# Optimization experiments

Hardware: AMD Instinct MI355X
Metric: run time of the kernel (lower is better)

## Reference

```python
import jax, jax.numpy as jnp
import numpy as np

D_MODEL, D_K, D_V, H, GRID = 512, 64, 64, 8, 196
B = 4


def setup_inputs() -> dict:
    key = jax.random.key(0)
    ks = jax.random.split(key, 12)
    s = 0.02
    return {
        "queries": jax.random.normal(ks[0], (B, GRID, D_MODEL), jnp.float32),
        "keys": jax.random.normal(ks[1], (B, GRID, D_MODEL), jnp.float32),
        "values": jax.random.normal(ks[2], (B, GRID, D_MODEL), jnp.float32),
        "Wq": jax.random.normal(ks[3], (H * D_K, D_MODEL), jnp.float32) * s,
        "bq": jnp.zeros((H * D_K,), jnp.float32),
        "Wk": jax.random.normal(ks[4], (H * D_K, D_MODEL), jnp.float32) * s,
        "bk": jnp.zeros((H * D_K,), jnp.float32),
        "Wv": jax.random.normal(ks[5], (H * D_V, D_MODEL), jnp.float32) * s,
        "bv": jnp.zeros((H * D_V,), jnp.float32),
        "Wo": jax.random.normal(ks[6], (D_MODEL, H * D_V), jnp.float32) * s,
        "bo": jnp.zeros((D_MODEL,), jnp.float32),
        "scale": jnp.ones((1, H, GRID, GRID), jnp.float32) / np.sqrt(D_K).astype(np.float32),
    }


def reference(queries, keys, values, Wq, bq, Wk, bk, Wv, bv, Wo, bo, scale):
    b, nq, _ = queries.shape
    nk = values.shape[1]
    # linear projections (torch nn.Linear: x @ W.T + b)
    q_sig = queries @ Wq.T + bq          # (b, nq, h*dk)
    k_p = keys @ Wk.T + bk               # (b, nk, h*dk)
    v_p = values @ Wv.T + bv             # (b, nk, h*dv)
    # elementwise q*k interaction (b, nq, nk, h*dk)
    att_e = q_sig[:, :, None, :] * k_p[:, None, :, :]
    # sigmoid-gated values
    v_g = jax.nn.sigmoid(att_e) * v_p[:, None, :, :]
    v = v_g.reshape(b, nq, nk, H, D_K).transpose(0, 3, 1, 2, 4)      # (b,h,nq,nk,dk)
    att = att_e.reshape(b, nq, nk, H, D_K).transpose(0, 3, 1, 2, 4)  # (b,h,nq,nk,dk)
    att = att.sum(-1) * scale            # (b,h,nq,nk)
    p = jax.nn.softmax(att, axis=-1)     # dropout is identity in eval mode
    # (att.unsqueeze(-2) @ v).squeeze(-2)
    image = jnp.einsum("bhqk,bhqkd->bhqd", p, v)
    image = image.transpose(0, 2, 1, 3).reshape(b, nq, H * D_V)
    out = image @ Wo.T + bo              # (b, nq, d_model)
    out = jax.nn.sigmoid(q_sig * out) * out
    return out
```

## Files before the change

kernel.cpp:

```cpp
#include <hip/hip_runtime.h>
#include <hip/hip_bf16.h>
#include <math.h>

#define NQ 196
#define BATCH 4
#define HD 512
#define NH 8
#define DK 64
#define MROWS 784
#define MPAD 832

typedef __attribute__((ext_vector_type(8))) short short8;
typedef __attribute__((ext_vector_type(4))) short short4v;
typedef __attribute__((ext_vector_type(4))) float float4v;

__device__ __forceinline__ float b2f(short s) {
  return __uint_as_float(((unsigned)(unsigned short)s) << 16);
}
__device__ __forceinline__ short f2b(float x) {
  return __builtin_bit_cast(short, __float2bfloat16(x));
}
__device__ __forceinline__ float fexp2(float x) {
  float r; asm("v_exp_f32 %0, %1" : "=v"(r) : "v"(x)); return r;
}
__device__ __forceinline__ float frcp(float x) {
  float r; asm("v_rcp_f32 %0, %1" : "=v"(r) : "v"(x)); return r;
}
__device__ __forceinline__ void cvt4(float4 v, short4v& hi, short4v& lo) {
  float x[4] = {v.x, v.y, v.z, v.w};
  #pragma unroll
  for (int i = 0; i < 4; ++i) {
    hi[i] = f2b(x[i]);
    lo[i] = f2b(x[i] - b2f(hi[i]));
  }
}
__device__ __forceinline__ void cvt8(float4 v0, float4 v1, short8& hi, short8& lo) {
  short4v h0, l0, h1, l1;
  cvt4(v0, h0, l0); cvt4(v1, h1, l1);
  hi = short8{h0[0],h0[1],h0[2],h0[3],h1[0],h1[1],h1[2],h1[3]};
  lo = short8{l0[0],l0[1],l0[2],l0[3],l1[0],l1[1],l1[2],l1[3]};
}
__device__ __forceinline__ void gload_lds16(const void* g, void* l) {
  __builtin_amdgcn_global_load_lds(
      (const __attribute__((address_space(1))) unsigned int*)g,
      (__attribute__((address_space(3))) unsigned int*)l, 16, 0, 0);
}

struct ProjArgs {
  const float* X[3]; const float* W[3]; const float* bias[3];
  float* Cf[3]; short* Ch[3]; short* Cl[3];
  const float* Wo; short* Woh; short* Wol;
};

__global__ __launch_bounds__(512)
void proj_kernel(ProjArgs a) {
  const int z = blockIdx.z;
  const float* __restrict__ X = a.X[z];
  const float* __restrict__ W = a.W[z];
  const int t = threadIdx.x;
  const int ln = t & 63, lm = ln & 15, quad = ln >> 4;
  const int w = t >> 6, wm = w >> 1, wn = w & 1;
  const int m0 = blockIdx.x << 6, n0 = blockIdx.y << 6;

  __shared__ __align__(16) short smem[32768];

  const int sr = t >> 3;
  const int cg = (t & 7) << 3;
  const int wIdx = sr * 64 + (cg ^ ((sr & 7) << 3));
  const float* gA = X + (size_t)min(m0 + sr, MROWS - 1) * HD;
  const float* gB = W + (size_t)(n0 + sr) * HD;

  float4 ra0, ra1, rb0, rb1;
  float4v acc0 = {0.f,0.f,0.f,0.f}, acc1 = {0.f,0.f,0.f,0.f};
  const int ar = (wm << 4) + lm;
  const int br0 = (wn << 5) + lm, br1 = br0 + 16;
  const int swz = (lm & 7) << 3;

  ra0 = *(const float4*)(gA + cg);     ra1 = *(const float4*)(gA + cg + 4);
  rb0 = *(const float4*)(gB + cg);     rb1 = *(const float4*)(gB + cg + 4);
  {
    short8 hi, lo;
    cvt8(ra0, ra1, hi, lo);
    *(short8*)&smem[0    + wIdx] = hi;  *(short8*)&smem[4096  + wIdx] = lo;
    cvt8(rb0, rb1, hi, lo);
    *(short8*)&smem[8192 + wIdx] = hi;  *(short8*)&smem[12288 + wIdx] = lo;
  }

  for (int kt = 0; kt < 8; ++kt) {
    const int buf = kt & 1;
    __syncthreads();
    if (kt < 7) {
      const int kb = (kt + 1) << 6;
      ra0 = *(const float4*)(gA + kb + cg);  ra1 = *(const float4*)(gA + kb + cg + 4);
      rb0 = *(const float4*)(gB + kb + cg);  rb1 = *(const float4*)(gB + kb + cg + 4);
    }
    const short* Sb = smem + (buf << 14);
    #pragma unroll
    for (int h2 = 0; h2 < 2; ++h2) {
      const int c = (h2 << 5) + (quad << 3);
      const int cs = c ^ swz;
      short8 a_h = *(const short8*)&Sb[         ar  * 64 + cs];
      short8 a_l = *(const short8*)&Sb[4096  +  ar  * 64 + cs];
      short8 b0h = *(const short8*)&Sb[8192  +  br0 * 64 + cs];
      short8 b0l = *(const short8*)&Sb[12288 +  br0 * 64 + cs];
      short8 b1h = *(const short8*)&Sb[8192  +  br1 * 64 + cs];
      short8 b1l = *(const short8*)&Sb[12288 +  br1 * 64 + cs];
      acc0 = __builtin_amdgcn_mfma_f32_16x16x32_bf16(a_h, b0h, acc0, 0,0,0);
      acc0 = __builtin_amdgcn_mfma_f32_16x16x32_bf16(a_h, b0l, acc0, 0,0,0);
      acc0 = __builtin_amdgcn_mfma_f32_16x16x32_bf16(a_l, b0h, acc0, 0,0,0);
      acc1 = __builtin_amdgcn_mfma_f32_16x16x32_bf16(a_h, b1h, acc1, 0,0,0);
      acc1 = __builtin_amdgcn_mfma_f32_16x16x32_bf16(a_h, b1l, acc1, 0,0,0);
      acc1 = __builtin_amdgcn_mfma_f32_16x16x32_bf16(a_l, b1h, acc1, 0,0,0);
    }
    if (kt < 7) {
      short* Nb = smem + ((buf ^ 1) << 14);
      short8 hi, lo;
      cvt8(ra0, ra1, hi, lo);
      *(short8*)&Nb[0    + wIdx] = hi;  *(short8*)&Nb[4096  + wIdx] = lo;
      cvt8(rb0, rb1, hi, lo);
      *(short8*)&Nb[8192 + wIdx] = hi;  *(short8*)&Nb[12288 + wIdx] = lo;
    }
  }

  {
    const float* bias = a.bias[z];
    float* Cf = a.Cf[z]; short* Ch = a.Ch[z]; short* Cl = a.Cl[z];
    #pragma unroll
    for (int nf = 0; nf < 2; ++nf) {
      const float4v av = nf ? acc1 : acc0;
      const int n = n0 + (wn << 5) + (nf << 4) + lm;
      const float bv = bias[n];
      #pragma unroll
      for (int r = 0; r < 4; ++r) {
        const int m = m0 + (wm << 4) + (quad << 2) + r;
        const float c = av[r] + bv;
        Cf[(size_t)m * HD + n] = c;
        if (Ch) {
          const short hi = f2b(c);
          Ch[(size_t)m * HD + n] = hi;
          Cl[(size_t)m * HD + n] = f2b(c - b2f(hi));
        }
      }
    }
  }

  if (z == 2) {
    const int lin = blockIdx.y * 13 + blockIdx.x;
    if (lin < 64) {
      const size_t off = (size_t)lin * 4096 + (size_t)t * 8;
      float4 v0 = *(const float4*)(a.Wo + off);
      float4 v1 = *(const float4*)(a.Wo + off + 4);
      short8 hi, lo; cvt8(v0, v1, hi, lo);
      *(short8*)(a.Woh + off) = hi;
      *(short8*)(a.Wol + off) = lo;
    }
  }
}

__global__ __launch_bounds__(512)
void attn_fused(const short* __restrict__ qsh, const short* __restrict__ qsl,
                const short* __restrict__ ksh, const short* __restrict__ ksl,
                const float* __restrict__ qsg, const float* __restrict__ kpg,
                const float* __restrict__ vpg, const float* __restrict__ scg,
                short* __restrict__ imgh, short* __restrict__ imgl) {
  const int q0 = blockIdx.x * 16;
  const int h  = blockIdx.y;
  const int b  = blockIdx.z;
  const int t  = threadIdx.x;
  const int w = t >> 6, ln = t & 63;
  const int lm = ln & 15, quad = ln >> 4;
  const float L2E = 1.4426950408889634f;

  __shared__ __align__(16) float S[16][212];
  __shared__ float R2[2][16][64];

  const size_t abase = ((size_t)(b * NQ) + q0 + lm) * HD + h * DK + (quad << 3);
  short8 ah0 = *(const short8*)(qsh + abase);
  short8 ah1 = *(const short8*)(qsh + abase + 32);
  short8 al0 = *(const short8*)(qsl + abase);
  short8 al1 = *(const short8*)(qsl + abase + 32);

  for (int nt = w; nt < 13; nt += 8) {
    const size_t bbase = ((size_t)(b * NQ) + nt * 16 + lm) * HD + h * DK + (quad << 3);
    short8 bh0 = *(const short8*)(ksh + bbase);
    short8 bh1 = *(const short8*)(ksh + bbase + 32);
    short8 bl0 = *(const short8*)(ksl + bbase);
    short8 bl1 = *(const short8*)(ksl + bbase + 32);
    float4v acc = {0.f, 0.f, 0.f, 0.f};
    acc = __builtin_amdgcn_mfma_f32_16x16x32_bf16(ah0, bh0, acc, 0,0,0);
    acc = __builtin_amdgcn_mfma_f32_16x16x32_bf16(ah1, bh1, acc, 0,0,0);
    acc = __builtin_amdgcn_mfma_f32_16x16x32_bf16(ah0, bl0, acc, 0,0,0);
    acc = __builtin_amdgcn_mfma_f32_16x16x32_bf16(ah1, bl1, acc, 0,0,0);
    acc = __builtin_amdgcn_mfma_f32_16x16x32_bf16(al0, bh0, acc, 0,0,0);
    acc = __builtin_amdgcn_mfma_f32_16x16x32_bf16(al1, bh1, acc, 0,0,0);
    #pragma unroll
    for (int r = 0; r < 4; ++r)
      S[(quad << 2) + r][nt * 16 + lm] = acc[r];
  }
  __syncthreads();

  for (int i = 0; i < 2; ++i) {
    const int rr = (w << 1) + i;
    const int q = q0 + rr;
    const bool qok = q < NQ;
    const float* srow = scg + ((size_t)h * NQ + (qok ? q : 0)) * NQ;
    float att[4];
    #pragma unroll
    for (int j = 0; j < 4; ++j) {
      const int c = ln + (j << 6);
      att[j] = -1e30f;
      if (c < NQ) att[j] = S[rr][c] * srow[c] * L2E;
    }
    float m = fmaxf(fmaxf(att[0], att[1]), fmaxf(att[2], att[3]));
    #pragma unroll
    for (int off = 32; off; off >>= 1) m = fmaxf(m, __shfl_xor(m, off, 64));
    float e[4], s = 0.f;
    #pragma unroll
    for (int j = 0; j < 4; ++j) { e[j] = fexp2(att[j] - m); s += e[j]; }
    #pragma unroll
    for (int off = 32; off; off >>= 1) s += __shfl_xor(s, off, 64);
    const float rinv = __fdividef(1.f, s);
    #pragma unroll
    for (int j = 0; j < 4; ++j) {
      const int c = ln + (j << 6);
      if (c < NQ) S[rr][c] = e[j] * rinv;
    }
  }
  __syncthreads();

  {
    const int d = ln;
    const int qg = (w >> 1) << 2;
    const int kh = w & 1;
    const int kbeg = kh ? 100 : 0;
    const int kend = kh ? 196 : 100;
    const float LOG2E = 1.4426950408889634f;

    float nqs[4];
    #pragma unroll
    for (int qi = 0; qi < 4; ++qi) {
      const int row = min(b * NQ + q0 + qg + qi, MROWS - 1);
      nqs[qi] = -qsg[(size_t)row * HD + h * DK + d] * LOG2E;
    }
    const float* kp = kpg + ((size_t)(b * NQ)) * HD + h * DK + d;
    const float* vp = vpg + ((size_t)(b * NQ)) * HD + h * DK + d;

    float acc[4] = {0.f, 0.f, 0.f, 0.f};

    for (int k = kbeg; k < kend; k += 4) {
      const float kv0 = kp[(size_t)(k + 0) * HD];
      const float kv1 = kp[(size_t)(k + 1) * HD];
      const float kv2 = kp[(size_t)(k + 2) * HD];
      const float kv3 = kp[(size_t)(k + 3) * HD];
      const float vv0 = vp[(size_t)(k + 0) * HD];
      const float vv1 = vp[(size_t)(k + 1) * HD];
      const float vv2 = vp[(size_t)(k + 2) * HD];
      const float vv3 = vp[(size_t)(k + 3) * HD];
      #pragma unroll
      for (int qi = 0; qi < 4; ++qi) {
        const float4 s4 = *(const float4*)&S[qg + qi][k];
        acc[qi] += s4.x * (vv0 * frcp(1.f + fexp2(nqs[qi] * kv0)));
        acc[qi] += s4.y * (vv1 * frcp(1.f + fexp2(nqs[qi] * kv1)));
        acc[qi] += s4.z * (vv2 * frcp(1.f + fexp2(nqs[qi] * kv2)));
        acc[qi] += s4.w * (vv3 * frcp(1.f + fexp2(nqs[qi] * kv3)));
      }
    }
    #pragma unroll
    for (int qi = 0; qi < 4; ++qi) R2[kh][qg + qi][d] = acc[qi];
  }
  __syncthreads();

  #pragma unroll
  for (int j = 0; j < 2; ++j) {
    const int idx = t + (j << 9);
    const int qi = idx >> 6, dd = idx & 63;
    const int q = q0 + qi;
    if (q < NQ) {
      const float s = R2[0][qi][dd] + R2[1][qi][dd];
      const size_t o = ((size_t)(b * NQ) + q) * HD + h * DK + dd;
      const short hi = f2b(s);
      imgh[o] = hi;
      imgl[o] = f2b(s - b2f(hi));
    }
  }
}

__global__ __launch_bounds__(512)
void out_kernel(const short* __restrict__ Ahp, const short* __restrict__ Alp,
                const short* __restrict__ Bhp, const short* __restrict__ Blp,
                const float* __restrict__ bo, const float* __restrict__ q_sig,
                float* __restrict__ out) {
  __shared__ short smem[24576];
  const int t = threadIdx.x;
  const int ln = t & 63, lm = ln & 15, quad = ln >> 4;
  const int w = t >> 6;
  const int wm = w >> 2, wn = w & 3;
  const int m0 = blockIdx.x << 5, n0 = blockIdx.y << 6;

  const int sr = t >> 3;
  const int sc = ((t & 7) ^ (sr & 7)) << 3;
  const short* gB_h = Bhp + (size_t)(n0 + sr) * HD + sc;
  const short* gB_l = Blp + (size_t)(n0 + sr) * HD + sc;
  const int tt = t & 255;
  const int ra = tt >> 3;
  const int sca = ((tt & 7) ^ (ra & 7)) << 3;
  const short* gA = ((t < 256) ? Ahp : Alp) + (size_t)(m0 + ra) * HD + sca;
  const int aoff = (t < 256) ? 0 : 2048;
  const int ldstA = aoff + tt * 8;
  const int ldstB = t * 8;

  float4v acc = {0.f,0.f,0.f,0.f};

  gload_lds16(gA,   &smem[ldstA]);
  gload_lds16(gB_h, &smem[4096 + ldstB]);
  gload_lds16(gB_l, &smem[8192 + ldstB]);

  const int ar = (wm << 4) + lm;
  const int br = (wn << 4) + lm;
  const int swz = (lm & 7) << 3;

  for (int kt = 0; kt < 8; ++kt) {
    const int buf = kt & 1;
    __syncthreads();
    if (kt < 7) {
      const int kb = (kt + 1) << 6;
      short* nb = &smem[(buf ^ 1) * 12288];
      gload_lds16(gA + kb,   &nb[ldstA]);
      gload_lds16(gB_h + kb, &nb[4096 + ldstB]);
      gload_lds16(gB_l + kb, &nb[8192 + ldstB]);
    }
    const short* Sb = &smem[buf * 12288];
    #pragma unroll
    for (int h2 = 0; h2 < 2; ++h2) {
      const int c = (h2 << 5) + (quad << 3);
      const int cs = c ^ swz;
      short8 a_h = *(const short8*)&Sb[         ar * 64 + cs];
      short8 a_l = *(const short8*)&Sb[2048  +  ar * 64 + cs];
      short8 b_h = *(const short8*)&Sb[4096  +  br * 64 + cs];
      short8 b_l = *(const short8*)&Sb[8192  +  br * 64 + cs];
      acc = __builtin_amdgcn_mfma_f32_16x16x32_bf16(a_h, b_h, acc, 0,0,0);
      acc = __builtin_amdgcn_mfma_f32_16x16x32_bf16(a_h, b_l, acc, 0,0,0);
      acc = __builtin_amdgcn_mfma_f32_16x16x32_bf16(a_l, b_h, acc, 0,0,0);
    }
  }

  {
    const int n = n0 + (wn << 4) + lm;
    const float bv = bo[n];
    #pragma unroll
    for (int r = 0; r < 4; ++r) {
      const int m = m0 + (wm << 4) + (quad << 2) + r;
      if (m < MROWS) {
        float c = acc[r] + bv;
        const float qg = q_sig[(size_t)m * HD + n];
        c = __fdividef(c, 1.f + __expf(-qg * c));
        out[(size_t)m * HD + n] = c;
      }
    }
  }
}

extern "C" void kernel_launch(void* const* d_in, const int* in_sizes, int n_in,
                              void* d_out, int out_size, void* d_ws, size_t ws_size,
                              hipStream_t stream) {
  const float* queries = (const float*)d_in[0];
  const float* keys    = (const float*)d_in[1];
  const float* values  = (const float*)d_in[2];
  const float* Wq = (const float*)d_in[3];
  const float* bq = (const float*)d_in[4];
  const float* Wk = (const float*)d_in[5];
  const float* bk = (const float*)d_in[6];
  const float* Wv = (const float*)d_in[7];
  const float* bv = (const float*)d_in[8];
  const float* Wo = (const float*)d_in[9];
  const float* bo = (const float*)d_in[10];
  const float* scale = (const float*)d_in[11];

  char* base = (char*)d_ws;
  const size_t NELPS = (size_t)MPAD * HD;
  const size_t WEL   = (size_t)HD * HD;

  size_t o = 0;
  float* q_sig = (float*)(base + o); o += NELPS * 4;
  float* k_p   = (float*)(base + o); o += NELPS * 4;
  float* v_p   = (float*)(base + o); o += NELPS * 4;
  short* qsh = (short*)(base + o); o += NELPS * 2;
  short* qsl = (short*)(base + o); o += NELPS * 2;
  short* ksh = (short*)(base + o); o += NELPS * 2;
  short* ksl = (short*)(base + o); o += NELPS * 2;
  short* imgh = (short*)(base + o); o += NELPS * 2;
  short* imgl = (short*)(base + o); o += NELPS * 2;
  short* Woh = (short*)(base + o); o += WEL * 2;
  short* Wol = (short*)(base + o); o += WEL * 2;

  ProjArgs p;
  p.X[0] = queries; p.X[1] = keys; p.X[2] = values;
  p.W[0] = Wq;      p.W[1] = Wk;   p.W[2] = Wv;
  p.bias[0] = bq;   p.bias[1] = bk; p.bias[2] = bv;
  p.Cf[0] = q_sig;  p.Cf[1] = k_p;  p.Cf[2] = v_p;
  p.Ch[0] = qsh; p.Cl[0] = qsl;
  p.Ch[1] = ksh; p.Cl[1] = ksl;
  p.Ch[2] = nullptr; p.Cl[2] = nullptr;
  p.Wo = Wo; p.Woh = Woh; p.Wol = Wol;
  proj_kernel<<<dim3(MPAD/64, HD/64, 3), 512, 0, stream>>>(p);

  attn_fused<<<dim3(13, NH, BATCH), 512, 0, stream>>>(
      qsh, qsl, ksh, ksl, q_sig, k_p, v_p, scale, imgh, imgl);

  out_kernel<<<dim3(MPAD/32, HD/64), 512, 0, stream>>>(
      imgh, imgl, Woh, Wol, bo, q_sig, (float*)d_out);
}
```

Measured before the change: 131.2 us.

## Deepen GEMM prefetch to two register stages and replace LDS-direct loads

The projection GEMM now keeps two register sets of global loads in flight, fully unrolls the K loop, and prefetches tiles two steps ahead so global latency overlaps with more MFMA work. The output GEMM drops global_load_lds direct-to-LDS loads in favour of register loads followed by swizzled LDS stores, using the same two-deep prefetch scheme. This raises register pressure and adds explicit LDS store instructions. It may also change how the compiler schedules waits around the barriers.

```diff
diff --git a/kernel.cpp b/kernel.cpp
--- a/kernel.cpp
+++ b/kernel.cpp
@@ -39,11 +39,6 @@
   cvt4(v0, h0, l0); cvt4(v1, h1, l1);
   hi = short8{h0[0],h0[1],h0[2],h0[3],h1[0],h1[1],h1[2],h1[3]};
   lo = short8{l0[0],l0[1],l0[2],l0[3],l1[0],l1[1],l1[2],l1[3]};
-}
-__device__ __forceinline__ void gload_lds16(const void* g, void* l) {
-  __builtin_amdgcn_global_load_lds(
-      (const __attribute__((address_space(1))) unsigned int*)g,
-      (__attribute__((address_space(3))) unsigned int*)l, 16, 0, 0);
 }
 
 struct ProjArgs {
@@ -70,57 +65,70 @@
   const float* gA = X + (size_t)min(m0 + sr, MROWS - 1) * HD;
   const float* gB = W + (size_t)(n0 + sr) * HD;
 
-  float4 ra0, ra1, rb0, rb1;
   float4v acc0 = {0.f,0.f,0.f,0.f}, acc1 = {0.f,0.f,0.f,0.f};
   const int ar = (wm << 4) + lm;
   const int br0 = (wn << 5) + lm, br1 = br0 + 16;
   const int swz = (lm & 7) << 3;
 
-  ra0 = *(const float4*)(gA + cg);     ra1 = *(const float4*)(gA + cg + 4);
-  rb0 = *(const float4*)(gB + cg);     rb1 = *(const float4*)(gB + cg + 4);
-  {
-    short8 hi, lo;
-    cvt8(ra0, ra1, hi, lo);
-    *(short8*)&smem[0    + wIdx] = hi;  *(short8*)&smem[4096  + wIdx] = lo;
-    cvt8(rb0, rb1, hi, lo);
-    *(short8*)&smem[8192 + wIdx] = hi;  *(short8*)&smem[12288 + wIdx] = lo;
-  }
-
-  for (int kt = 0; kt < 8; ++kt) {
-    const int buf = kt & 1;
+  float4 a0A, a1A, b0A, b1A;
+  float4 a0B, a1B, b0B, b1B;
+
+#define PLOADA(T) do { const int kb = (T) << 6; \
+    a0A = *(const float4*)(gA + kb + cg);  a1A = *(const float4*)(gA + kb + cg + 4); \
+    b0A = *(const float4*)(gB + kb + cg);  b1A = *(const float4*)(gB + kb + cg + 4); } while(0)
+#define PLOADB(T) do { const int kb = (T) << 6; \
+    a0B = *(const float4*)(gA + kb + cg);  a1B = *(const float4*)(gA + kb + cg + 4); \
+    b0B = *(const float4*)(gB + kb + cg);  b1B = *(const float4*)(gB + kb + cg + 4); } while(0)
+#define PSTAGEA(BUF) do { short8 hi, lo; \
+    cvt8(a0A, a1A, hi, lo); \
+    *(short8*)&smem[(BUF) + 0    + wIdx] = hi;  *(short8*)&smem[(BUF) + 4096  + wIdx] = lo; \
+    cvt8(b0A, b1A, hi, lo); \
+    *(short8*)&smem[(BUF) + 8192 + wIdx] = hi;  *(short8*)&smem[(BUF) + 12288 + wIdx] = lo; } while(0)
+#define PSTAGEB(BUF) do { short8 hi, lo; \
+    cvt8(a0B, a1B, hi, lo); \
+    *(short8*)&smem[(BUF) + 0    + wIdx] = hi;  *(short8*)&smem[(BUF) + 4096  + wIdx] = lo; \
+    cvt8(b0B, b1B, hi, lo); \
+    *(short8*)&smem[(BUF) + 8192 + wIdx] = hi;  *(short8*)&smem[(BUF) + 12288 + wIdx] = lo; } while(0)
+#define PMFMA(BUF) do { const short* Sb = smem + (BUF); \
+    _Pragma("unroll") \
+    for (int h2 = 0; h2 < 2; ++h2) { \
+      const int c = (h2 << 5) + (quad << 3); \
+      const int cs = c ^ swz; \
+      short8 a_h = *(const short8*)&Sb[         ar  * 64 + cs]; \
+      short8 a_l = *(const short8*)&Sb[4096  +  ar  * 64 + cs]; \
+      short8 b0h = *(const short8*)&Sb[8192  +  br0 * 64 + cs]; \
+      short8 b0l = *(const short8*)&Sb[12288 +  br0 * 64 + cs]; \
+      short8 b1h = *(const short8*)&Sb[8192  +  br1 * 64 + cs]; \
+      short8 b1l = *(const short8*)&Sb[12288 +  br1 * 64 + cs]; \
+      acc0 = __builtin_amdgcn_mfma_f32_16x16x32_bf16(a_h, b0h, acc0, 0,0,0); \
+      acc0 = __builtin_amdgcn_mfma_f32_16x16x32_bf16(a_h, b0l, acc0, 0,0,0); \
+      acc0 = __builtin_amdgcn_mfma_f32_16x16x32_bf16(a_l, b0h, acc0, 0,0,0); \
+      acc1 = __builtin_amdgcn_mfma_f32_16x16x32_bf16(a_h, b1h, acc1, 0,0,0); \
+      acc1 = __builtin_amdgcn_mfma_f32_16x16x32_bf16(a_h, b1l, acc1, 0,0,0); \
+      acc1 = __builtin_amdgcn_mfma_f32_16x16x32_bf16(a_l, b1h, acc1, 0,0,0); \
+    } } while(0)
+
+  PLOADA(0);
+  PSTAGEA(0);
+  PLOADB(1);
+
+  #pragma unroll
+  for (int kk = 0; kk < 4; ++kk) {
+    const int kt = kk << 1;
     __syncthreads();
-    if (kt < 7) {
-      const int kb = (kt + 1) << 6;
-      ra0 = *(const float4*)(gA + kb + cg);  ra1 = *(const float4*)(gA + kb + cg + 4);
-      rb0 = *(const float4*)(gB + kb + cg);  rb1 = *(const float4*)(gB + kb + cg + 4);
-    }
-    const short* Sb = smem + (buf << 14);
-    #pragma unroll
-    for (int h2 = 0; h2 < 2; ++h2) {
-      const int c = (h2 << 5) + (quad << 3);
-      const int cs = c ^ swz;
-      short8 a_h = *(const short8*)&Sb[         ar  * 64 + cs];
-      short8 a_l = *(const short8*)&Sb[4096  +  ar  * 64 + cs];
-      short8 b0h = *(const short8*)&Sb[8192  +  br0 * 64 + cs];
-      short8 b0l = *(const short8*)&Sb[12288 +  br0 * 64 + cs];
-      short8 b1h = *(const short8*)&Sb[8192  +  br1 * 64 + cs];
-      short8 b1l = *(const short8*)&Sb[12288 +  br1 * 64 + cs];
-      acc0 = __builtin_amdgcn_mfma_f32_16x16x32_bf16(a_h, b0h, acc0, 0,0,0);
-      acc0 = __builtin_amdgcn_mfma_f32_16x16x32_bf16(a_h, b0l, acc0, 0,0,0);
-      acc0 = __builtin_amdgcn_mfma_f32_16x16x32_bf16(a_l, b0h, acc0, 0,0,0);
-      acc1 = __builtin_amdgcn_mfma_f32_16x16x32_bf16(a_h, b1h, acc1, 0,0,0);
-      acc1 = __builtin_amdgcn_mfma_f32_16x16x32_bf16(a_h, b1l, acc1, 0,0,0);
-      acc1 = __builtin_amdgcn_mfma_f32_16x16x32_bf16(a_l, b1h, acc1, 0,0,0);
-    }
-    if (kt < 7) {
-      short* Nb = smem + ((buf ^ 1) << 14);
-      short8 hi, lo;
-      cvt8(ra0, ra1, hi, lo);
-      *(short8*)&Nb[0    + wIdx] = hi;  *(short8*)&Nb[4096  + wIdx] = lo;
-      cvt8(rb0, rb1, hi, lo);
-      *(short8*)&Nb[8192 + wIdx] = hi;  *(short8*)&Nb[12288 + wIdx] = lo;
-    }
-  }
+    if (kt + 2 < 8) PLOADA(kt + 2);
+    PMFMA(0);
+    if (kt + 1 < 8) PSTAGEB(16384);
+    __syncthreads();
+    if (kt + 3 < 8) PLOADB(kt + 3);
+    PMFMA(16384);
+    if (kt + 2 < 8) PSTAGEA(0);
+  }
+#undef PLOADA
+#undef PLOADB
+#undef PSTAGEA
+#undef PSTAGEB
+#undef PMFMA
 
   {
     const float* bias = a.bias[z];
@@ -290,59 +298,83 @@
                 const short* __restrict__ Bhp, const short* __restrict__ Blp,
                 const float* __restrict__ bo, const float* __restrict__ q_sig,
                 float* __restrict__ out) {
-  __shared__ short smem[24576];
+  __shared__ __align__(16) short smem[24576];
   const int t = threadIdx.x;
   const int ln = t & 63, lm = ln & 15, quad = ln >> 4;
   const int w = t >> 6;
   const int wm = w >> 2, wn = w & 3;
   const int m0 = blockIdx.x << 5, n0 = blockIdx.y << 6;
 
+  const int ra = (t & 255) >> 3;
+  const int cga = (t & 7) << 3;
+  const int aBase = (t < 256) ? 0 : 2048;
+  const int wIdxA = aBase + ra * 64 + (cga ^ ((ra & 7) << 3));
+  const short* gAs = ((t < 256) ? Ahp : Alp) + (size_t)(m0 + ra) * HD + cga;
+
   const int sr = t >> 3;
-  const int sc = ((t & 7) ^ (sr & 7)) << 3;
-  const short* gB_h = Bhp + (size_t)(n0 + sr) * HD + sc;
-  const short* gB_l = Blp + (size_t)(n0 + sr) * HD + sc;
-  const int tt = t & 255;
-  const int ra = tt >> 3;
-  const int sca = ((tt & 7) ^ (ra & 7)) << 3;
-  const short* gA = ((t < 256) ? Ahp : Alp) + (size_t)(m0 + ra) * HD + sca;
-  const int aoff = (t < 256) ? 0 : 2048;
-  const int ldstA = aoff + tt * 8;
-  const int ldstB = t * 8;
-
-  float4v acc = {0.f,0.f,0.f,0.f};
-
-  gload_lds16(gA,   &smem[ldstA]);
-  gload_lds16(gB_h, &smem[4096 + ldstB]);
-  gload_lds16(gB_l, &smem[8192 + ldstB]);
+  const int cgb = (t & 7) << 3;
+  const int wIdxB = sr * 64 + (cgb ^ ((sr & 7) << 3));
+  const short* gBh = Bhp + (size_t)(n0 + sr) * HD + cgb;
+  const short* gBl = Blp + (size_t)(n0 + sr) * HD + cgb;
 
   const int ar = (wm << 4) + lm;
   const int br = (wn << 4) + lm;
   const int swz = (lm & 7) << 3;
 
-  for (int kt = 0; kt < 8; ++kt) {
-    const int buf = kt & 1;
+  float4v acc = {0.f,0.f,0.f,0.f};
+  short8 laA, lbhA, lblA, laB, lbhB, lblB;
+
+#define OLOADA(T) do { const int kb = (T) << 6; \
+    laA  = *(const short8*)(gAs + kb); \
+    lbhA = *(const short8*)(gBh + kb); \
+    lblA = *(const short8*)(gBl + kb); } while(0)
+#define OLOADB(T) do { const int kb = (T) << 6; \
+    laB  = *(const short8*)(gAs + kb); \
+    lbhB = *(const short8*)(gBh + kb); \
+    lblB = *(const short8*)(gBl + kb); } while(0)
+#define OSTAGEA(BUF) do { \
+    *(short8*)&smem[(BUF) + wIdxA] = laA; \
+    *(short8*)&smem[(BUF) + 4096 + wIdxB] = lbhA; \
+    *(short8*)&smem[(BUF) + 8192 + wIdxB] = lblA; } while(0)
+#define OSTAGEB(BUF) do { \
+    *(short8*)&smem[(BUF) + wIdxA] = laB; \
+    *(short8*)&smem[(BUF) + 4096 + wIdxB] = lbhB; \
+    *(short8*)&smem[(BUF) + 8192 + wIdxB] = lblB; } while(0)
+#define OMFMA(BUF) do { const short* Sb = &smem[(BUF)]; \
+    _Pragma("unroll") \
+    for (int h2 = 0; h2 < 2; ++h2) { \
+      const int c = (h2 << 5) + (quad << 3); \
+      const int cs = c ^ swz; \
+      short8 a_h = *(const short8*)&Sb[         ar * 64 + cs]; \
+      short8 a_l = *(const short8*)&Sb[2048  +  ar * 64 + cs]; \
+      short8 b_h = *(const short8*)&Sb[4096  +  br * 64 + cs]; \
+      short8 b_l = *(const short8*)&Sb[8192  +  br * 64 + cs]; \
+      acc = __builtin_amdgcn_mfma_f32_16x16x32_bf16(a_h, b_h, acc, 0,0,0); \
+      acc = __builtin_amdgcn_mfma_f32_16x16x32_bf16(a_h, b_l, acc, 0,0,0); \
+      acc = __builtin_amdgcn_mfma_f32_16x16x32_bf16(a_l, b_h, acc, 0,0,0); \
+    } } while(0)
+
+  OLOADA(0);
+  OSTAGEA(0);
+  OLOADB(1);
+
+  #pragma unroll
+  for (int kk = 0; kk < 4; ++kk) {
+    const int kt = kk << 1;
     __syncthreads();
-    if (kt < 7) {
-      const int kb = (kt + 1) << 6;
-      short* nb = &smem[(buf ^ 1) * 12288];
-      gload_lds16(gA + kb,   &nb[ldstA]);
-      gload_lds16(gB_h + kb, &nb[4096 + ldstB]);
-      gload_lds16(gB_l + kb, &nb[8192 + ldstB]);
-    }
-    const short* Sb = &smem[buf * 12288];
-    #pragma unroll
-    for (int h2 = 0; h2 < 2; ++h2) {
-      const int c = (h2 << 5) + (quad << 3);
-      const int cs = c ^ swz;
-      short8 a_h = *(const short8*)&Sb[         ar * 64 + cs];
-      short8 a_l = *(const short8*)&Sb[2048  +  ar * 64 + cs];
-      short8 b_h = *(const short8*)&Sb[4096  +  br * 64 + cs];
-      short8 b_l = *(const short8*)&Sb[8192  +  br * 64 + cs];
-      acc = __builtin_amdgcn_mfma_f32_16x16x32_bf16(a_h, b_h, acc, 0,0,0);
-      acc = __builtin_amdgcn_mfma_f32_16x16x32_bf16(a_h, b_l, acc, 0,0,0);
-      acc = __builtin_amdgcn_mfma_f32_16x16x32_bf16(a_l, b_h, acc, 0,0,0);
-    }
-  }
+    if (kt + 2 < 8) OLOADA(kt + 2);
+    OMFMA(0);
+    if (kt + 1 < 8) OSTAGEB(12288);
+    __syncthreads();
+    if (kt + 3 < 8) OLOADB(kt + 3);
+    OMFMA(12288);
+    if (kt + 2 < 8) OSTAGEA(0);
+  }
+#undef OLOADA
+#undef OLOADB
+#undef OSTAGEA
+#undef OSTAGEB
+#undef OMFMA
 
   {
     const int n = n0 + (wn << 4) + lm;
```

Result: no change. 131.7 us (+0.4%).

## Shrink projection GEMM tiles and use 256-thread attention blocks without key split

Applied to the files above, without the earlier changes.

The projection GEMM now uses 32x64 tiles with one 16x16 accumulator per wave, which doubles the grid to raise occupancy on the 784x512 problems. The attention kernel drops to 4 waves of 256 threads. Each wave owns 4 query rows and the full key range, so the R2 cross-wave reduction and two barriers go away. This trades per-block parallelism and longer serial per-thread loops in the sigmoid-gated accumulation for less synchronization and shared memory, and adds more redundant K/V loads across projection tiles.

```diff
diff --git a/kernel.cpp b/kernel.cpp
--- a/kernel.cpp
+++ b/kernel.cpp
@@ -59,93 +59,92 @@
   const float* __restrict__ W = a.W[z];
   const int t = threadIdx.x;
   const int ln = t & 63, lm = ln & 15, quad = ln >> 4;
-  const int w = t >> 6, wm = w >> 1, wn = w & 1;
-  const int m0 = blockIdx.x << 6, n0 = blockIdx.y << 6;
-
-  __shared__ __align__(16) short smem[32768];
-
+  const int w = t >> 6, wm = w >> 2, wn = w & 3;
+  const int m0 = blockIdx.x << 5, n0 = blockIdx.y << 6;
+
+  __shared__ __align__(16) short smem[24576];
+
+  const bool aload = t < 256;
+  const int ra = (t & 255) >> 3;
+  const int cga = (t & 7) << 3;
+  const int wIdxA = ra * 64 + (cga ^ ((ra & 7) << 3));
+  const float* gA = X + (size_t)min(m0 + ra, MROWS - 1) * HD;
   const int sr = t >> 3;
-  const int cg = (t & 7) << 3;
-  const int wIdx = sr * 64 + (cg ^ ((sr & 7) << 3));
-  const float* gA = X + (size_t)min(m0 + sr, MROWS - 1) * HD;
+  const int cgb = (t & 7) << 3;
+  const int wIdxB = sr * 64 + (cgb ^ ((sr & 7) << 3));
   const float* gB = W + (size_t)(n0 + sr) * HD;
 
   float4 ra0, ra1, rb0, rb1;
-  float4v acc0 = {0.f,0.f,0.f,0.f}, acc1 = {0.f,0.f,0.f,0.f};
+  float4v acc = {0.f,0.f,0.f,0.f};
   const int ar = (wm << 4) + lm;
-  const int br0 = (wn << 5) + lm, br1 = br0 + 16;
+  const int br = (wn << 4) + lm;
   const int swz = (lm & 7) << 3;
 
-  ra0 = *(const float4*)(gA + cg);     ra1 = *(const float4*)(gA + cg + 4);
-  rb0 = *(const float4*)(gB + cg);     rb1 = *(const float4*)(gB + cg + 4);
+  if (aload) { ra0 = *(const float4*)(gA + cga);  ra1 = *(const float4*)(gA + cga + 4); }
+  rb0 = *(const float4*)(gB + cgb);  rb1 = *(const float4*)(gB + cgb + 4);
   {
     short8 hi, lo;
-    cvt8(ra0, ra1, hi, lo);
-    *(short8*)&smem[0    + wIdx] = hi;  *(short8*)&smem[4096  + wIdx] = lo;
+    if (aload) {
+      cvt8(ra0, ra1, hi, lo);
+      *(short8*)&smem[0 + wIdxA] = hi;  *(short8*)&smem[2048 + wIdxA] = lo;
+    }
     cvt8(rb0, rb1, hi, lo);
-    *(short8*)&smem[8192 + wIdx] = hi;  *(short8*)&smem[12288 + wIdx] = lo;
+    *(short8*)&smem[4096 + wIdxB] = hi;  *(short8*)&smem[8192 + wIdxB] = lo;
   }
 
   for (int kt = 0; kt < 8; ++kt) {
-    const int buf = kt & 1;
+    const int buf = (kt & 1) * 12288;
     __syncthreads();
     if (kt < 7) {
       const int kb = (kt + 1) << 6;
-      ra0 = *(const float4*)(gA + kb + cg);  ra1 = *(const float4*)(gA + kb + cg + 4);
-      rb0 = *(const float4*)(gB + kb + cg);  rb1 = *(const float4*)(gB + kb + cg + 4);
-    }
-    const short* Sb = smem + (buf << 14);
+      if (aload) { ra0 = *(const float4*)(gA + kb + cga);  ra1 = *(const float4*)(gA + kb + cga + 4); }
+      rb0 = *(const float4*)(gB + kb + cgb);  rb1 = *(const float4*)(gB + kb + cgb + 4);
+    }
+    const short* Sb = smem + buf;
     #pragma unroll
     for (int h2 = 0; h2 < 2; ++h2) {
       const int c = (h2 << 5) + (quad << 3);
       const int cs = c ^ swz;
-      short8 a_h = *(const short8*)&Sb[         ar  * 64 + cs];
-      short8 a_l = *(const short8*)&Sb[4096  +  ar  * 64 + cs];
-      short8 b0h = *(const short8*)&Sb[8192  +  br0 * 64 + cs];
-      short8 b0l = *(const short8*)&Sb[12288 +  br0 * 64 + cs];
-      short8 b1h = *(const short8*)&Sb[8192  +  br1 * 64 + cs];
-      short8 b1l = *(const short8*)&Sb[12288 +  br1 * 64 + cs];
-      acc0 = __builtin_amdgcn_mfma_f32_16x16x32_bf16(a_h, b0h, acc0, 0,0,0);
-      acc0 = __builtin_amdgcn_mfma_f32_16x16x32_bf16(a_h, b0l, acc0, 0,0,0);
-      acc0 = __builtin_amdgcn_mfma_f32_16x16x32_bf16(a_l, b0h, acc0, 0,0,0);
-      acc1 = __builtin_amdgcn_mfma_f32_16x16x32_bf16(a_h, b1h, acc1, 0,0,0);
-      acc1 = __builtin_amdgcn_mfma_f32_16x16x32_bf16(a_h, b1l, acc1, 0,0,0);
-      acc1 = __builtin_amdgcn_mfma_f32_16x16x32_bf16(a_l, b1h, acc1, 0,0,0);
+      short8 a_h = *(const short8*)&Sb[         ar * 64 + cs];
+      short8 a_l = *(const short8*)&Sb[2048  +  ar * 64 + cs];
+      short8 b_h = *(const short8*)&Sb[4096  +  br * 64 + cs];
+      short8 b_l = *(const short8*)&Sb[8192  +  br * 64 + cs];
+      acc = __builtin_amdgcn_mfma_f32_16x16x32_bf16(a_h, b_h, acc, 0,0,0);
+      acc = __builtin_amdgcn_mfma_f32_16x16x32_bf16(a_h, b_l, acc, 0,0,0);
+      acc = __builtin_amdgcn_mfma_f32_16x16x32_bf16(a_l, b_h, acc, 0,0,0);
     }
     if (kt < 7) {
-      short* Nb = smem + ((buf ^ 1) << 14);
+      short* Nb = smem + (buf ^ 12288);
       short8 hi, lo;
-      cvt8(ra0, ra1, hi, lo);
-      *(short8*)&Nb[0    + wIdx] = hi;  *(short8*)&Nb[4096  + wIdx] = lo;
+      if (aload) {
+        cvt8(ra0, ra1, hi, lo);
+        *(short8*)&Nb[0 + wIdxA] = hi;  *(short8*)&Nb[2048 + wIdxA] = lo;
+      }
       cvt8(rb0, rb1, hi, lo);
-      *(short8*)&Nb[8192 + wIdx] = hi;  *(short8*)&Nb[12288 + wIdx] = lo;
+      *(short8*)&Nb[4096 + wIdxB] = hi;  *(short8*)&Nb[8192 + wIdxB] = lo;
     }
   }
 
   {
     const float* bias = a.bias[z];
     float* Cf = a.Cf[z]; short* Ch = a.Ch[z]; short* Cl = a.Cl[z];
-    #pragma unroll
-    for (int nf = 0; nf < 2; ++nf) {
-      const float4v av = nf ? acc1 : acc0;
-      const int n = n0 + (wn << 5) + (nf << 4) + lm;
-      const float bv = bias[n];
-      #pragma unroll
-      for (int r = 0; r < 4; ++r) {
-        const int m = m0 + (wm << 4) + (quad << 2) + r;
-        const float c = av[r] + bv;
-        Cf[(size_t)m * HD + n] = c;
-        if (Ch) {
-          const short hi = f2b(c);
-          Ch[(size_t)m * HD + n] = hi;
-          Cl[(size_t)m * HD + n] = f2b(c - b2f(hi));
-        }
+    const int n = n0 + (wn << 4) + lm;
+    const float bv = bias[n];
+    #pragma unroll
+    for (int r = 0; r < 4; ++r) {
+      const int m = m0 + (wm << 4) + (quad << 2) + r;
+      const float c = acc[r] + bv;
+      Cf[(size_t)m * HD + n] = c;
+      if (Ch) {
+        const short hi = f2b(c);
+        Ch[(size_t)m * HD + n] = hi;
+        Cl[(size_t)m * HD + n] = f2b(c - b2f(hi));
       }
     }
   }
 
   if (z == 2) {
-    const int lin = blockIdx.y * 13 + blockIdx.x;
+    const int lin = blockIdx.y * 26 + blockIdx.x;
     if (lin < 64) {
       const size_t off = (size_t)lin * 4096 + (size_t)t * 8;
       float4 v0 = *(const float4*)(a.Wo + off);
@@ -157,7 +156,7 @@
   }
 }
 
-__global__ __launch_bounds__(512)
+__global__ __launch_bounds__(256)
 void attn_fused(const short* __restrict__ qsh, const short* __restrict__ qsl,
                 const short* __restrict__ ksh, const short* __restrict__ ksl,
                 const float* __restrict__ qsg, const float* __restrict__ kpg,
@@ -172,7 +171,6 @@
   const float L2E = 1.4426950408889634f;
 
   __shared__ __align__(16) float S[16][212];
-  __shared__ float R2[2][16][64];
 
   const size_t abase = ((size_t)(b * NQ) + q0 + lm) * HD + h * DK + (quad << 3);
   short8 ah0 = *(const short8*)(qsh + abase);
@@ -180,7 +178,7 @@
   short8 al0 = *(const short8*)(qsl + abase);
   short8 al1 = *(const short8*)(qsl + abase + 32);
 
-  for (int nt = w; nt < 13; nt += 8) {
+  for (int nt = w; nt < 13; nt += 4) {
     const size_t bbase = ((size_t)(b * NQ) + nt * 16 + lm) * HD + h * DK + (quad << 3);
     short8 bh0 = *(const short8*)(ksh + bbase);
     short8 bh1 = *(const short8*)(ksh + bbase + 32);
@@ -199,8 +197,9 @@
   }
   __syncthreads();
 
-  for (int i = 0; i < 2; ++i) {
-    const int rr = (w << 1) + i;
+  #pragma unroll
+  for (int i = 0; i < 4; ++i) {
+    const int rr = (w << 2) + i;
     const int q = q0 + rr;
     const bool qok = q < NQ;
     const float* srow = scg + ((size_t)h * NQ + (qok ? q : 0)) * NQ;
@@ -226,14 +225,10 @@
       if (c < NQ) S[rr][c] = e[j] * rinv;
     }
   }
-  __syncthreads();
 
   {
     const int d = ln;
-    const int qg = (w >> 1) << 2;
-    const int kh = w & 1;
-    const int kbeg = kh ? 100 : 0;
-    const int kend = kh ? 196 : 100;
+    const int qg = w << 2;
     const float LOG2E = 1.4426950408889634f;
 
     float nqs[4];
@@ -247,7 +242,7 @@
 
     float acc[4] = {0.f, 0.f, 0.f, 0.f};
 
-    for (int k = kbeg; k < kend; k += 4) {
+    for (int k = 0; k < NQ; k += 4) {
       const float kv0 = kp[(size_t)(k + 0) * HD];
       const float kv1 = kp[(size_t)(k + 1) * HD];
       const float kv2 = kp[(size_t)(k + 2) * HD];
@@ -265,22 +260,16 @@
         acc[qi] += s4.w * (vv3 * frcp(1.f + fexp2(nqs[qi] * kv3)));
       }
     }
-    #pragma unroll
-    for (int qi = 0; qi < 4; ++qi) R2[kh][qg + qi][d] = acc[qi];
-  }
-  __syncthreads();
-
-  #pragma unroll
-  for (int j = 0; j < 2; ++j) {
-    const int idx = t + (j << 9);
-    const int qi = idx >> 6, dd = idx & 63;
-    const int q = q0 + qi;
-    if (q < NQ) {
-      const float s = R2[0][qi][dd] + R2[1][qi][dd];
-      const size_t o = ((size_t)(b * NQ) + q) * HD + h * DK + dd;
-      const short hi = f2b(s);
-      imgh[o] = hi;
-      imgl[o] = f2b(s - b2f(hi));
+
+    #pragma unroll
+    for (int qi = 0; qi < 4; ++qi) {
+      const int q = q0 + qg + qi;
+      if (q < NQ) {
+        const size_t o = ((size_t)(b * NQ) + q) * HD + h * DK + d;
+        const short hi = f2b(acc[qi]);
+        imgh[o] = hi;
+        imgl[o] = f2b(acc[qi] - b2f(hi));
+      }
     }
   }
 }
@@ -402,9 +391,9 @@
   p.Ch[1] = ksh; p.Cl[1] = ksl;
   p.Ch[2] = nullptr; p.Cl[2] = nullptr;
   p.Wo = Wo; p.Woh = Woh; p.Wol = Wol;
-  proj_kernel<<<dim3(MPAD/64, HD/64, 3), 512, 0, stream>>>(p);
-
-  attn_fused<<<dim3(13, NH, BATCH), 512, 0, stream>>>(
+  proj_kernel<<<dim3(MPAD/32, HD/64, 3), 512, 0, stream>>>(p);
+
+  attn_fused<<<dim3(13, NH, BATCH), 256, 0, stream>>>(
       qsh, qsl, ksh, ksl, q_sig, k_p, v_p, scale, imgh, imgl);
 
   out_kernel<<<dim3(MPAD/32, HD/64), 512, 0, stream>>>(
```

New measurement: 138.6 us. 5.6% more time.
